# Performance work log

Hardware: AMD Instinct MI355X
Metric: run time of the kernel (lower is better)

## Reference

```python
import jax, jax.numpy as jnp
import numpy as np
from jax import lax

D_MODEL = 768
D_INNER = 1536   # expand * d_model
D_STATE = 16
D_CONV = 4
DT_RANK = 48     # ceil(768/16)
BATCH, SEQLEN = 2, 1024


def silu(x):
    return x * jax.nn.sigmoid(x)


def causal_conv1d(x, w, b):
    # x: (B, L, d)  w: (d, K) depthwise  b: (d,)
    # matches torch Conv1d(groups=d, padding=K-1)[..., :L]
    K = w.shape[1]
    L = x.shape[1]
    xp = jnp.pad(x, ((0, 0), (K - 1, 0), (0, 0)))
    out = b
    for k in range(K):
        out = out + xp[:, k:k + L, :] * w[:, k]
    return out


def mamba_branch(xz, conv_w, conv_b, x_proj_w, dt_proj_w, dt_bias, A_log, D):
    # xz: (B, L, 2*d_inner); faithful to mamba_inner_fn_no_out_proj
    x, z = jnp.split(xz, 2, axis=-1)
    x = silu(causal_conv1d(x, conv_w, conv_b))
    x_dbl = x @ x_proj_w.T                                  # (B,L,dt_rank+2N)
    dt, Bc, Cc = jnp.split(x_dbl, [DT_RANK, DT_RANK + D_STATE], axis=-1)
    delta = jax.nn.softplus(dt @ dt_proj_w.T + dt_bias)     # (B,L,d)
    A = -jnp.exp(A_log)                                     # (d,N)
    dA = jnp.exp(delta[..., None] * A)                      # (B,L,d,N)
    dBx = (delta * x)[..., None] * Bc[:, :, None, :]        # (B,L,d,N)

    def step(h, inp):
        da, dbx = inp
        h = da * h + dbx
        return h, h

    h0 = jnp.zeros((x.shape[0], x.shape[2], D_STATE), x.dtype)
    _, hs = lax.scan(step, h0, (jnp.swapaxes(dA, 0, 1), jnp.swapaxes(dBx, 0, 1)))
    y = jnp.einsum('lbdn,bln->bld', hs, Cc) + x * D         # (B,L,d)
    return y * silu(z)


def setup_inputs() -> dict:
    key = jax.random.key(0)
    ks = jax.random.split(key, 16)
    d, dm, n, r, K = D_INNER, D_MODEL, D_STATE, DT_RANK, D_CONV
    A_log = jnp.log(jnp.broadcast_to(jnp.arange(1, n + 1, dtype=jnp.float32), (d, n)))
    # faithful dt bias init: inverse-softplus of log-uniform dt in [1e-3, 1e-1]
    def dt_bias(k):
        dt = jnp.exp(jax.random.uniform(k, (d,)) * (np.log(0.1) - np.log(0.001)) + np.log(0.001))
        dt = jnp.clip(dt, 1e-4)
        return dt + jnp.log(-jnp.expm1(-dt))
    return {
        'hidden_states': jax.random.normal(ks[0], (BATCH, SEQLEN, dm), jnp.float32),
        'in_proj_w': jax.random.normal(ks[1], (2 * d, dm), jnp.float32) / np.sqrt(dm),
        'conv_w': jax.random.normal(ks[2], (d, K), jnp.float32) / np.sqrt(K),
        'conv_b': jax.random.normal(ks[3], (d,), jnp.float32) * 0.02,
        'x_proj_w': jax.random.normal(ks[4], (r + 2 * n, d), jnp.float32) / np.sqrt(d),
        'dt_proj_w': jax.random.uniform(ks[5], (d, r), jnp.float32, -r ** -0.5, r ** -0.5),
        'dt_proj_b': dt_bias(ks[6]),
        'A_log': A_log,
        'D': jnp.ones((d,), jnp.float32),
        'conv_w_b': jax.random.normal(ks[7], (d, K), jnp.float32) / np.sqrt(K),
        'conv_b_b': jax.random.normal(ks[8], (d,), jnp.float32) * 0.02,
        'x_proj_w_b': jax.random.normal(ks[9], (r + 2 * n, d), jnp.float32) / np.sqrt(d),
        'dt_proj_w_b': jax.random.uniform(ks[10], (d, r), jnp.float32, -r ** -0.5, r ** -0.5),
        'dt_proj_b_b': dt_bias(ks[11]),
        'A_b_log': A_log,
        'D_b': jnp.ones((d,), jnp.float32),
        'out_proj_w': jax.random.normal(ks[12], (dm, d), jnp.float32) / np.sqrt(d),
    }


def reference(hidden_states, in_proj_w, conv_w, conv_b, x_proj_w, dt_proj_w, dt_proj_b,
              A_log, D, conv_w_b, conv_b_b, x_proj_w_b, dt_proj_w_b, dt_proj_b_b,
              A_b_log, D_b, out_proj_w):
    # bimamba v2: forward scan + backward (flipped) scan, summed, then out_proj
    xz = hidden_states @ in_proj_w.T                        # (B,L,2*d_inner)
    out_f = mamba_branch(xz, conv_w, conv_b, x_proj_w, dt_proj_w, dt_proj_b, A_log, D)
    out_r = mamba_branch(xz[:, ::-1, :], conv_w_b, conv_b_b, x_proj_w_b,
                         dt_proj_w_b, dt_proj_b_b, A_b_log, D_b)[:, ::-1, :]
    return (out_f + out_r) @ out_proj_w.T                   # (B,L,d_model)
```

## Files before the change

kernel.cpp:

```cpp
#include <hip/hip_runtime.h>
#include <hip/hip_bf16.h>

#define LL 1024
#define DI 1536
#define N2 3072
#define ML 2048

typedef __attribute__((ext_vector_type(8))) short short8;
typedef __attribute__((ext_vector_type(4))) float f4;
typedef __attribute__((ext_vector_type(4))) float f32x4;

__device__ __forceinline__ ushort f2bf(float f) {
  union { float f; unsigned u; } v; v.f = f;
  unsigned u = v.u;
  u += 0x7fffu + ((u >> 16) & 1u);
  return (ushort)(u >> 16);
}
__device__ __forceinline__ float bf2f(ushort u) {
  union { unsigned i; float f; } w; w.i = ((unsigned)u) << 16; return w.f;
}
__device__ __forceinline__ f4 bf2f4(ushort4 u) {
  f4 r; r.x = bf2f(u.x); r.y = bf2f(u.y); r.z = bf2f(u.z); r.w = bf2f(u.w);
  return r;
}

__device__ __forceinline__ void gload16(const ushort* g, ushort* l) {
  __builtin_amdgcn_global_load_lds(
      (const __attribute__((address_space(1))) unsigned int*)g,
      (__attribute__((address_space(3))) unsigned int*)l, 16, 0, 0);
}

struct CvtSeg { const float* s; ushort* d; int n4; };
struct Cvt5 { CvtSeg seg[5]; };

#define CVT_BLOCKS 5232

__global__ void k_cvt(Cvt5 p, int total4,
                      const float* __restrict__ wf, const float* __restrict__ wb,
                      ushort* __restrict__ dtw) {
  int bid = blockIdx.x;
  if (bid < CVT_BLOCKS) {
    int i = bid * 256 + threadIdx.x;
    if (i >= total4) return;
    int off = i, sidx = 0;
    while (sidx < 4 && off >= p.seg[sidx].n4) { off -= p.seg[sidx].n4; ++sidx; }
    f4 v = *(const f4*)(p.seg[sidx].s + (size_t)off * 4);
    ushort4 o;
    o.x = f2bf(v.x); o.y = f2bf(v.y); o.z = f2bf(v.z); o.w = f2bf(v.w);
    *(ushort4*)(p.seg[sidx].d + (size_t)off * 4) = o;
  } else {
    int i = (bid - CVT_BLOCKS) * 256 + threadIdx.x;
    int c = i & 63;
    int rr = i >> 6;
    int dir = rr / 1536;
    int r = rr - dir * 1536;
    const float* w = dir ? wb : wf;
    dtw[i] = (c < 48) ? f2bf(w[r * 48 + c]) : (ushort)0;
  }
}

template<int EPI, bool NGUARD, int KS, bool OBF>
__global__ __launch_bounds__(256)
void k_gemm(const ushort* __restrict__ A, const ushort* __restrict__ Bm,
            void* __restrict__ Cp, int M, int N, int K,
            const float* __restrict__ bias, const float* __restrict__ bias2,
            size_t sA, size_t sB, size_t sC, size_t sKs, int kLen) {
  const int dir = blockIdx.z;
  A += (size_t)dir * sA;
  Bm += (size_t)dir * sB;
  size_t cbase = (size_t)dir * sC;
  const float* bp = (EPI == 1) ? (dir ? bias2 : bias) : nullptr;

  int n0, kOff, kEnd;
  if (KS > 1) {
    int yb_ = blockIdx.y;
    int nt = yb_ / KS, ks = yb_ - nt * KS;
    n0 = nt * 128;
    kOff = ks * kLen;
    kEnd = kOff + kLen;
    cbase += (size_t)ks * sKs;
  } else {
    n0 = blockIdx.y * 128;
    kOff = 0;
    kEnd = K;
  }

  __shared__ ushort As[128 * 32];
  __shared__ ushort Bs[128 * 32];
  const int tid = threadIdx.x;
  const int m0 = blockIdx.x * 128;
  const int wv = tid >> 6;
  const int lane = tid & 63;
  const int wr = (wv >> 1) * 64;
  const int wc = (wv & 1) * 64;
  const int lr = lane & 15;
  const int lk = lane >> 4;
  f32x4 acc[4][4] = {};
  for (int k0 = kOff; k0 < kEnd; k0 += 32) {
    #pragma unroll
    for (int i = 0; i < 2; ++i) {
      int e = (tid + i * 256) * 8;
      int r = e >> 5;
      int c = e & 31;
      gload16(A + (size_t)(m0 + r) * K + k0 + c, &As[(i * 256 + wv * 64) * 8]);
      gload16(Bm + (size_t)(n0 + r) * K + k0 + c, &Bs[(i * 256 + wv * 64) * 8]);
    }
    __syncthreads();
    short8 af[4], bfr[4];
    #pragma unroll
    for (int m = 0; m < 4; ++m) af[m] = *(const short8*)(&As[(wr + m*16 + lr) * 32 + lk*8]);
    #pragma unroll
    for (int n = 0; n < 4; ++n) bfr[n] = *(const short8*)(&Bs[(wc + n*16 + lr) * 32 + lk*8]);
    #pragma unroll
    for (int m = 0; m < 4; ++m)
      #pragma unroll
      for (int n = 0; n < 4; ++n)
        acc[m][n] = __builtin_amdgcn_mfma_f32_16x16x32_bf16(af[m], bfr[n], acc[m][n], 0, 0, 0);
    __syncthreads();
  }
  #pragma unroll
  for (int m = 0; m < 4; ++m) {
    int gr = m0 + wr + m * 16 + lk * 4;
    #pragma unroll
    for (int n = 0; n < 4; ++n) {
      int gc = n0 + wc + n * 16 + lr;
      if (NGUARD && gc >= N) continue;
      #pragma unroll
      for (int r = 0; r < 4; ++r) {
        float v = acc[m][n][r];
        if (EPI == 1) {
          v += bp[gc];
          v = (v > 20.f) ? v : log1pf(__expf(v));
        }
        size_t idx = cbase + (size_t)(gr + r) * N + gc;
        if (OBF) ((ushort*)Cp)[idx] = f2bf(v);
        else     ((float*)Cp)[idx] = v;
      }
    }
  }
}

__global__ void k_xred(const float* __restrict__ partial,
                       float* __restrict__ dtBC, ushort* __restrict__ dtbf) {
  int i = blockIdx.x * 256 + threadIdx.x;
  int dir = i / 40960;
  int rem = i - dir * 40960;
  int row = rem / 20;
  int c4 = rem - row * 20;
  f4 s = {0.f, 0.f, 0.f, 0.f};
  #pragma unroll
  for (int ks = 0; ks < 8; ++ks) {
    f4 v = *(const f4*)(partial + (((size_t)(dir * 8 + ks) * 2048 + row) * 80 + c4 * 4));
    s.x += v.x; s.y += v.y; s.z += v.z; s.w += v.w;
  }
  *(f4*)(dtBC + ((size_t)dir * 163840 + (size_t)row * 80 + c4 * 4)) = s;
  if (c4 < 16) {
    ushort4 u;
    if (c4 < 12) { u.x = f2bf(s.x); u.y = f2bf(s.y); u.z = f2bf(s.z); u.w = f2bf(s.w); }
    else { u.x = 0; u.y = 0; u.z = 0; u.w = 0; }
    *(ushort4*)(dtbf + ((size_t)dir * 131072 + (size_t)row * 64 + c4 * 4)) = u;
  }
}

__global__ void k_ored(const float* __restrict__ part, float* __restrict__ out) {
  int i = blockIdx.x * 256 + threadIdx.x;
  f4 s = {0.f, 0.f, 0.f, 0.f};
  #pragma unroll
  for (int ks = 0; ks < 4; ++ks) {
    f4 v = *(const f4*)(part + (size_t)ks * 1572864 + (size_t)i * 4);
    s.x += v.x; s.y += v.y; s.z += v.z; s.w += v.w;
  }
  *(f4*)(out + (size_t)i * 4) = s;
}

#define CONV_R 8
__global__ __launch_bounds__(192)
void k_conv2(const ushort* __restrict__ xz,
             const float* __restrict__ wf, const float* __restrict__ bf_,
             const float* __restrict__ wb, const float* __restrict__ bb_,
             ushort* __restrict__ xcbf) {
  int d4 = blockIdx.z * 192 + threadIdx.x;
  int b = blockIdx.y;
  int l0 = blockIdx.x * CONV_R;
  int d = d4 * 4;
  f4 w0[4], w1[4];
  #pragma unroll
  for (int c = 0; c < 4; ++c) {
    w0[c] = *(const f4*)(wf + (size_t)d * 4 + c * 4);
    w1[c] = *(const f4*)(wb + (size_t)d * 4 + c * 4);
  }
  f4 bias0 = *(const f4*)(bf_ + d);
  f4 bias1 = *(const f4*)(bb_ + d);
  f4 win[CONV_R + 6];
  #pragma unroll
  for (int j = 0; j < CONV_R + 6; ++j) {
    int t = l0 - 3 + j;
    if (t >= 0 && t < LL) {
      win[j] = bf2f4(*(const ushort4*)(xz + ((size_t)(b * LL + t)) * N2 + d));
    } else {
      f4 z = {0.f, 0.f, 0.f, 0.f};
      win[j] = z;
    }
  }
  #pragma unroll
  for (int i = 0; i < CONV_R; ++i) {
    int l = l0 + i;
    float a0[4], a1[4];
    #pragma unroll
    for (int c = 0; c < 4; ++c) { a0[c] = bias0[c]; a1[c] = bias1[c]; }
    #pragma unroll
    for (int k = 0; k < 4; ++k) {
      f4 xv0 = win[i + k];
      f4 xv1 = win[i + 3 + k];
      #pragma unroll
      for (int c = 0; c < 4; ++c) {
        a0[c] += xv0[c] * w0[c][k];
        a1[c] += xv1[c] * w1[c][3 - k];
      }
    }
    ushort4 o0, o1;
    #pragma unroll
    for (int c = 0; c < 4; ++c) {
      a0[c] = a0[c] / (1.f + __expf(-a0[c]));
      a1[c] = a1[c] / (1.f + __expf(-a1[c]));
    }
    o0.x = f2bf(a0[0]); o0.y = f2bf(a0[1]); o0.z = f2bf(a0[2]); o0.w = f2bf(a0[3]);
    o1.x = f2bf(a1[0]); o1.y = f2bf(a1[1]); o1.z = f2bf(a1[2]); o1.w = f2bf(a1[3]);
    *(ushort4*)(xcbf + ((size_t)(b * LL + l)) * DI + d) = o0;
    *(ushort4*)(xcbf + ((size_t)(ML + b * LL + (LL - 1 - l))) * DI + d) = o1;
  }
}

__global__ __launch_bounds__(256)
void k_scan1(const ushort* __restrict__ delta_all,
             const ushort* __restrict__ xc_all,
             const float* __restrict__ dtBC_all,
             const float* __restrict__ Alog_f, const float* __restrict__ Alog_b,
             float* __restrict__ hL, float* __restrict__ P) {
  int dirb = blockIdx.z;
  int dir = dirb >> 1, b = dirb & 1;
  int ch = blockIdx.y;
  int d = blockIdx.x * 256 + threadIdx.x;
  const float* Alog = dir ? Alog_b : Alog_f;
  float Av[16];
  #pragma unroll
  for (int n = 0; n < 16; ++n) Av[n] = -__expf(Alog[d * 16 + n]);
  int l0 = ch * 32;
  size_t base = ((size_t)dir * ML + (size_t)b * LL + l0) * DI + d;
  const ushort* dptr = delta_all + base;
  const ushort* xptr = xc_all + base;
  const float* bc = dtBC_all + ((size_t)dir * ML + (size_t)b * LL + l0) * 80 + 48;
  float h[16];
  #pragma unroll
  for (int n = 0; n < 16; ++n) h[n] = 0.f;
  float s = 0.f;
  for (int l = 0; l < 32; ++l) {
    float dl = bf2f(dptr[(size_t)l * DI]);
    float xv = bf2f(xptr[(size_t)l * DI]);
    float dbx = dl * xv;
    s += dl;
    const float* bp = bc + l * 80;
    #pragma unroll
    for (int q = 0; q < 4; ++q) {
      f4 Bv = *(const f4*)(bp + q * 4);
      #pragma unroll
      for (int j = 0; j < 4; ++j) {
        int n = q * 4 + j;
        h[n] = __expf(dl * Av[n]) * h[n] + dbx * Bv[j];
      }
    }
  }
  size_t si = (((size_t)dirb * 32 + ch) * 1536 + d) * 16;
  #pragma unroll
  for (int q = 0; q < 4; ++q) {
    f4 hv = {h[q*4], h[q*4+1], h[q*4+2], h[q*4+3]};
    f4 pv = {__expf(Av[q*4] * s), __expf(Av[q*4+1] * s),
             __expf(Av[q*4+2] * s), __expf(Av[q*4+3] * s)};
    *(f4*)(hL + si + q * 4) = hv;
    *(f4*)(P + si + q * 4) = pv;
  }
}

__global__ void k_comb(const float* __restrict__ hL, const float* __restrict__ P,
                       float* __restrict__ hIn) {
  int tid = blockIdx.x * 256 + threadIdx.x;
  int dirb = tid / 24576;
  int e = tid - dirb * 24576;
  size_t base = (size_t)dirb * 786432 + e;
  float h = 0.f;
  #pragma unroll
  for (int ch = 0; ch < 32; ++ch) {
    hIn[base + (size_t)ch * 24576] = h;
    h = P[base + (size_t)ch * 24576] * h + hL[base + (size_t)ch * 24576];
  }
}

__global__ __launch_bounds__(256)
void k_scan2(const ushort* __restrict__ delta_all,
             const ushort* __restrict__ xc_all,
             const float* __restrict__ dtBC_all,
             const float* __restrict__ Alog_f, const float* __restrict__ Df,
             const float* __restrict__ Alog_b, const float* __restrict__ Db,
             const float* __restrict__ hIn,
             ushort* __restrict__ yf, ushort* __restrict__ yb) {
  int dirb = blockIdx.z;
  int dir = dirb >> 1, b = dirb & 1;
  int ch = blockIdx.y;
  int d = blockIdx.x * 256 + threadIdx.x;
  const float* Alog = dir ? Alog_b : Alog_f;
  const float* Dp = dir ? Db : Df;
  float Av[16];
  #pragma unroll
  for (int n = 0; n < 16; ++n) Av[n] = -__expf(Alog[d * 16 + n]);
  float Dvv = Dp[d];
  int l0 = ch * 32;
  size_t base = ((size_t)dir * ML + (size_t)b * LL + l0) * DI + d;
  const ushort* dptr = delta_all + base;
  const ushort* xptr = xc_all + base;
  const float* bc = dtBC_all + ((size_t)dir * ML + (size_t)b * LL + l0) * 80 + 48;
  ushort* yo = dir ? yb : yf;
  size_t si = (((size_t)dirb * 32 + ch) * 1536 + d) * 16;
  float h[16];
  #pragma unroll
  for (int q = 0; q < 4; ++q) {
    f4 hv = *(const f4*)(hIn + si + q * 4);
    h[q*4] = hv.x; h[q*4+1] = hv.y; h[q*4+2] = hv.z; h[q*4+3] = hv.w;
  }
  for (int l = 0; l < 32; ++l) {
    float dl = bf2f(dptr[(size_t)l * DI]);
    float xv = bf2f(xptr[(size_t)l * DI]);
    float dbx = dl * xv;
    const float* bp = bc + l * 80;
    float pr0 = 0.f, pr1 = 0.f, pr2 = 0.f, pr3 = 0.f;
    #pragma unroll
    for (int q = 0; q < 4; ++q) {
      f4 Bv = *(const f4*)(bp + q * 4);
      f4 Cv = *(const f4*)(bp + 16 + q * 4);
      float pq = 0.f;
      #pragma unroll
      for (int j = 0; j < 4; ++j) {
        int n = q * 4 + j;
        h[n] = __expf(dl * Av[n]) * h[n] + dbx * Bv[j];
        pq += h[n] * Cv[j];
      }
      if (q == 0) pr0 = pq; else if (q == 1) pr1 = pq;
      else if (q == 2) pr2 = pq; else pr3 = pq;
    }
    float pr = (pr0 + pr1) + (pr2 + pr3);
    int gl = l0 + l;
    int lo = dir ? (LL - 1 - gl) : gl;
    yo[((size_t)b * LL + lo) * DI + d] = f2bf(pr + xv * Dvv);
  }
}

__global__ void k_gate(const ushort* __restrict__ a, const ushort* __restrict__ b,
                       const ushort* __restrict__ xz, ushort* __restrict__ o) {
  int i = blockIdx.x * 256 + threadIdx.x;
  int row = i / 384;
  int c4 = i - row * 384;
  f4 va = bf2f4(*(const ushort4*)(a + (size_t)i * 4));
  f4 vb = bf2f4(*(const ushort4*)(b + (size_t)i * 4));
  f4 vz = bf2f4(*(const ushort4*)(xz + (size_t)row * N2 + DI + c4 * 4));
  ushort4 u;
  float s0 = vz.x / (1.f + __expf(-vz.x));
  float s1 = vz.y / (1.f + __expf(-vz.y));
  float s2 = vz.z / (1.f + __expf(-vz.z));
  float s3 = vz.w / (1.f + __expf(-vz.w));
  u.x = f2bf((va.x + vb.x) * s0);
  u.y = f2bf((va.y + vb.y) * s1);
  u.z = f2bf((va.z + vb.z) * s2);
  u.w = f2bf((va.w + vb.w) * s3);
  *(ushort4*)(o + (size_t)i * 4) = u;
}

extern "C" void kernel_launch(void* const* d_in, const int* in_sizes, int n_in,
                              void* d_out, int out_size, void* d_ws, size_t ws_size,
                              hipStream_t stream) {
  const float* hidden      = (const float*)d_in[0];
  const float* in_proj_w   = (const float*)d_in[1];
  const float* conv_w      = (const float*)d_in[2];
  const float* conv_b      = (const float*)d_in[3];
  const float* x_proj_w    = (const float*)d_in[4];
  const float* dt_proj_w   = (const float*)d_in[5];
  const float* dt_proj_b   = (const float*)d_in[6];
  const float* A_log       = (const float*)d_in[7];
  const float* Dv          = (const float*)d_in[8];
  const float* conv_w_b    = (const float*)d_in[9];
  const float* conv_b_b    = (const float*)d_in[10];
  const float* x_proj_w_b  = (const float*)d_in[11];
  const float* dt_proj_w_b = (const float*)d_in[12];
  const float* dt_proj_b_b = (const float*)d_in[13];
  const float* A_b_log     = (const float*)d_in[14];
  const float* D_b         = (const float*)d_in[15];
  const float* out_proj_w  = (const float*)d_in[16];
  float* out = (float*)d_out;

  float* wsf   = (float*)d_ws;
  float* dtBC  = wsf;
  float* hL    = wsf + 327680;
  float* P     = wsf + 3473408;
  float* hIn   = wsf + 6619136;
  float* xpart = wsf + 327680;
  float* opart = wsf + 327680;
  ushort* wsb      = (ushort*)((char*)d_ws + 39059456);
  ushort* hid_bf   = wsb;
  ushort* win_bf   = wsb + 1572864;
  ushort* xw_bf    = wsb + 3932160;
  ushort* dtw_bf   = wsb + 4177920;
  ushort* wout_bf  = wsb + 4374528;
  ushort* xz_bf    = wsb + 5554176;
  ushort* xc_bf    = wsb + 11845632;
  ushort* dt_bf    = wsb + 18137088;
  ushort* delta_bf = wsb + 18399232;
  ushort* ybf_f    = wsb + 24690688;
  ushort* ybf_b    = wsb + 27836416;
  ushort* y_bf     = wsb + 30982144;
  if (ws_size < 107315200) return;

  Cvt5 c5;
  c5.seg[0] = { hidden,      hid_bf,            1572864 / 4 };
  c5.seg[1] = { in_proj_w,   win_bf,            2359296 / 4 };
  c5.seg[2] = { x_proj_w,    xw_bf,             122880 / 4 };
  c5.seg[3] = { x_proj_w_b,  xw_bf + 122880,    122880 / 4 };
  c5.seg[4] = { out_proj_w,  wout_bf,           1179648 / 4 };
  k_cvt<<<CVT_BLOCKS + 768, 256, 0, stream>>>(c5, 1339392, dt_proj_w, dt_proj_w_b, dtw_bf);

  k_gemm<0, false, 1, true><<<dim3(16, 24), 256, 0, stream>>>(
      hid_bf, win_bf, xz_bf, 2048, 3072, 768, nullptr, nullptr, 0, 0, 0, 0, 0);

  k_conv2<<<dim3(LL / CONV_R, 2, 2), 192, 0, stream>>>(
      xz_bf, conv_w, conv_b, conv_w_b, conv_b_b, xc_bf);

  k_gemm<0, true, 8, false><<<dim3(16, 8, 2), 256, 0, stream>>>(
      xc_bf, xw_bf, xpart, 2048, 80, 1536, nullptr, nullptr,
      3145728, 122880, 1310720, 163840, 192);
  k_xred<<<320, 256, 0, stream>>>(xpart, dtBC, dt_bf);

  k_gemm<1, false, 1, true><<<dim3(16, 12, 2), 256, 0, stream>>>(
      dt_bf, dtw_bf, delta_bf, 2048, 1536, 64, dt_proj_b, dt_proj_b_b,
      131072, 98304, 3145728, 0, 0);

  k_scan1<<<dim3(6, 32, 4), 256, 0, stream>>>(delta_bf, xc_bf, dtBC, A_log, A_b_log, hL, P);
  k_comb<<<384, 256, 0, stream>>>(hL, P, hIn);
  k_scan2<<<dim3(6, 32, 4), 256, 0, stream>>>(delta_bf, xc_bf, dtBC,
                                              A_log, Dv, A_b_log, D_b, hIn, ybf_f, ybf_b);

  k_gate<<<3072, 256, 0, stream>>>(ybf_f, ybf_b, xz_bf, y_bf);

  k_gemm<0, false, 4, false><<<dim3(16, 24), 256, 0, stream>>>(
      y_bf, wout_bf, opart, 2048, 768, 1536, nullptr, nullptr,
      0, 0, 0, 1572864, 384);
  k_ored<<<1536, 256, 0, stream>>>(opart, out);
}
```

Measured before the change: 278.2 us.

## Double scan chunk count, store per-chunk delta sums, prefetch scan inputs

Splits the sequence into 64 chunks of 16 instead of 32 chunks of 32, doubling the number of scan blocks to raise GPU occupancy and shorten each block's serial dependency chain. Scan1 now writes only the per-channel delta sum instead of a 16-wide decay product array, and the combine kernel recomputes the decay with an exp from A_log. The scan loops also prefetch the next delta and x values and are unrolled by 4. In exchange, the hL/hIn state buffers double in size, the combine pass becomes a longer serial loop, and the workspace grows.

```diff
diff --git a/kernel.cpp b/kernel.cpp
--- a/kernel.cpp
+++ b/kernel.cpp
@@ -5,6 +5,8 @@
 #define DI 1536
 #define N2 3072
 #define ML 2048
+#define CHUNKS 64
+#define CLEN 16
 
 typedef __attribute__((ext_vector_type(8))) short short8;
 typedef __attribute__((ext_vector_type(4))) float f4;
@@ -236,7 +238,7 @@
              const ushort* __restrict__ xc_all,
              const float* __restrict__ dtBC_all,
              const float* __restrict__ Alog_f, const float* __restrict__ Alog_b,
-             float* __restrict__ hL, float* __restrict__ P) {
+             float* __restrict__ hL, float* __restrict__ Sv) {
   int dirb = blockIdx.z;
   int dir = dirb >> 1, b = dirb & 1;
   int ch = blockIdx.y;
@@ -245,7 +247,7 @@
   float Av[16];
   #pragma unroll
   for (int n = 0; n < 16; ++n) Av[n] = -__expf(Alog[d * 16 + n]);
-  int l0 = ch * 32;
+  int l0 = ch * CLEN;
   size_t base = ((size_t)dir * ML + (size_t)b * LL + l0) * DI + d;
   const ushort* dptr = delta_all + base;
   const ushort* xptr = xc_all + base;
@@ -254,9 +256,15 @@
   #pragma unroll
   for (int n = 0; n < 16; ++n) h[n] = 0.f;
   float s = 0.f;
-  for (int l = 0; l < 32; ++l) {
-    float dl = bf2f(dptr[(size_t)l * DI]);
-    float xv = bf2f(xptr[(size_t)l * DI]);
+  ushort dln = dptr[0], xvn = xptr[0];
+  #pragma unroll 4
+  for (int l = 0; l < CLEN; ++l) {
+    float dl = bf2f(dln);
+    float xv = bf2f(xvn);
+    if (l + 1 < CLEN) {
+      dln = dptr[(size_t)(l + 1) * DI];
+      xvn = xptr[(size_t)(l + 1) * DI];
+    }
     float dbx = dl * xv;
     s += dl;
     const float* bp = bc + l * 80;
@@ -270,28 +278,32 @@
       }
     }
   }
-  size_t si = (((size_t)dirb * 32 + ch) * 1536 + d) * 16;
+  size_t si = (((size_t)dirb * CHUNKS + ch) * 1536 + d) * 16;
   #pragma unroll
   for (int q = 0; q < 4; ++q) {
     f4 hv = {h[q*4], h[q*4+1], h[q*4+2], h[q*4+3]};
-    f4 pv = {__expf(Av[q*4] * s), __expf(Av[q*4+1] * s),
-             __expf(Av[q*4+2] * s), __expf(Av[q*4+3] * s)};
     *(f4*)(hL + si + q * 4) = hv;
-    *(f4*)(P + si + q * 4) = pv;
-  }
-}
-
-__global__ void k_comb(const float* __restrict__ hL, const float* __restrict__ P,
+  }
+  Sv[((size_t)dirb * CHUNKS + ch) * 1536 + d] = s;
+}
+
+__global__ void k_comb(const float* __restrict__ hL, const float* __restrict__ Sv,
+                       const float* __restrict__ Alog_f, const float* __restrict__ Alog_b,
                        float* __restrict__ hIn) {
   int tid = blockIdx.x * 256 + threadIdx.x;
   int dirb = tid / 24576;
   int e = tid - dirb * 24576;
-  size_t base = (size_t)dirb * 786432 + e;
+  int d = e >> 4;
+  const float* Alog = (dirb >> 1) ? Alog_b : Alog_f;
+  float Av = -__expf(Alog[e]);
+  size_t hbase = (size_t)dirb * CHUNKS * 24576 + e;
+  size_t sbase = (size_t)dirb * CHUNKS * 1536 + d;
   float h = 0.f;
-  #pragma unroll
-  for (int ch = 0; ch < 32; ++ch) {
-    hIn[base + (size_t)ch * 24576] = h;
-    h = P[base + (size_t)ch * 24576] * h + hL[base + (size_t)ch * 24576];
+  #pragma unroll 8
+  for (int ch = 0; ch < CHUNKS; ++ch) {
+    hIn[hbase + (size_t)ch * 24576] = h;
+    float Pv = __expf(Av * Sv[sbase + (size_t)ch * 1536]);
+    h = Pv * h + hL[hbase + (size_t)ch * 24576];
   }
 }
 
@@ -313,22 +325,28 @@
   #pragma unroll
   for (int n = 0; n < 16; ++n) Av[n] = -__expf(Alog[d * 16 + n]);
   float Dvv = Dp[d];
-  int l0 = ch * 32;
+  int l0 = ch * CLEN;
   size_t base = ((size_t)dir * ML + (size_t)b * LL + l0) * DI + d;
   const ushort* dptr = delta_all + base;
   const ushort* xptr = xc_all + base;
   const float* bc = dtBC_all + ((size_t)dir * ML + (size_t)b * LL + l0) * 80 + 48;
   ushort* yo = dir ? yb : yf;
-  size_t si = (((size_t)dirb * 32 + ch) * 1536 + d) * 16;
+  size_t si = (((size_t)dirb * CHUNKS + ch) * 1536 + d) * 16;
   float h[16];
   #pragma unroll
   for (int q = 0; q < 4; ++q) {
     f4 hv = *(const f4*)(hIn + si + q * 4);
     h[q*4] = hv.x; h[q*4+1] = hv.y; h[q*4+2] = hv.z; h[q*4+3] = hv.w;
   }
-  for (int l = 0; l < 32; ++l) {
-    float dl = bf2f(dptr[(size_t)l * DI]);
-    float xv = bf2f(xptr[(size_t)l * DI]);
+  ushort dln = dptr[0], xvn = xptr[0];
+  #pragma unroll 4
+  for (int l = 0; l < CLEN; ++l) {
+    float dl = bf2f(dln);
+    float xv = bf2f(xvn);
+    if (l + 1 < CLEN) {
+      dln = dptr[(size_t)(l + 1) * DI];
+      xvn = xptr[(size_t)(l + 1) * DI];
+    }
     float dbx = dl * xv;
     const float* bp = bc + l * 80;
     float pr0 = 0.f, pr1 = 0.f, pr2 = 0.f, pr3 = 0.f;
@@ -398,11 +416,11 @@
   float* wsf   = (float*)d_ws;
   float* dtBC  = wsf;
   float* hL    = wsf + 327680;
-  float* P     = wsf + 3473408;
-  float* hIn   = wsf + 6619136;
+  float* Sv    = wsf + 6619136;
+  float* hIn   = wsf + 7012352;
   float* xpart = wsf + 327680;
   float* opart = wsf + 327680;
-  ushort* wsb      = (ushort*)((char*)d_ws + 39059456);
+  ushort* wsb      = (ushort*)((char*)d_ws + 53215232);
   ushort* hid_bf   = wsb;
   ushort* win_bf   = wsb + 1572864;
   ushort* xw_bf    = wsb + 3932160;
@@ -415,7 +433,7 @@
   ushort* ybf_f    = wsb + 24690688;
   ushort* ybf_b    = wsb + 27836416;
   ushort* y_bf     = wsb + 30982144;
-  if (ws_size < 107315200) return;
+  if (ws_size < 121470976) return;
 
   Cvt5 c5;
   c5.seg[0] = { hidden,      hid_bf,            1572864 / 4 };
@@ -440,10 +458,11 @@
       dt_bf, dtw_bf, delta_bf, 2048, 1536, 64, dt_proj_b, dt_proj_b_b,
       131072, 98304, 3145728, 0, 0);
 
-  k_scan1<<<dim3(6, 32, 4), 256, 0, stream>>>(delta_bf, xc_bf, dtBC, A_log, A_b_log, hL, P);
-  k_comb<<<384, 256, 0, stream>>>(hL, P, hIn);
-  k_scan2<<<dim3(6, 32, 4), 256, 0, stream>>>(delta_bf, xc_bf, dtBC,
-                                              A_log, Dv, A_b_log, D_b, hIn, ybf_f, ybf_b);
+  k_scan1<<<dim3(6, CHUNKS, 4), 256, 0, stream>>>(delta_bf, xc_bf, dtBC,
+                                                  A_log, A_b_log, hL, Sv);
+  k_comb<<<384, 256, 0, stream>>>(hL, Sv, A_log, A_b_log, hIn);
+  k_scan2<<<dim3(6, CHUNKS, 4), 256, 0, stream>>>(delta_bf, xc_bf, dtBC,
+                                                  A_log, Dv, A_b_log, D_b, hIn, ybf_f, ybf_b);
 
   k_gate<<<3072, 256, 0, stream>>>(ybf_f, ybf_b, xz_bf, y_bf);
 
```

Result: faster. 262.3 us (-5.7%).
